# Optimization experiments

Measured on AMD Instinct MI355X. Metric: run time of the kernel, lower is better.

## Reference

```python
import jax, jax.numpy as jnp
import numpy as np

HIDDEN = 896
NUM_Q_HEADS = 14
NUM_KV_HEADS = 2
HEAD_DIM = 64
ROPE_BASE = 10000.0
B, S = 4, 2048


def rotate_half(x):
    x1, x2 = jnp.split(x, 2, axis=-1)
    return jnp.concatenate((-x2, x1), axis=-1)


def rope_cos_sin(position_ids):
    # position_ids: [B, S] int -> cos/sin [B, 1, S, HEAD_DIM]
    inv_freq = 1.0 / (ROPE_BASE ** (jnp.arange(0, HEAD_DIM, 2, dtype=jnp.float32) / HEAD_DIM))
    freqs = position_ids.astype(jnp.float32)[..., None] * inv_freq  # [B,S,D/2]
    emb = jnp.concatenate((freqs, freqs), axis=-1)  # [B,S,D]
    return jnp.cos(emb)[:, None, :, :], jnp.sin(emb)[:, None, :, :]


def setup_inputs() -> dict:
    key = jax.random.key(0)
    k1, k2, k3, k4, k5 = jax.random.split(key, 5)
    s = 1.0 / np.sqrt(HIDDEN)
    return {
        "hidden_states": jax.random.normal(k1, (B, S, HIDDEN), dtype=jnp.float32),
        "position_ids": jnp.broadcast_to(jnp.arange(S, dtype=jnp.int64), (B, S)),
        "Wq": jax.random.normal(k2, (HIDDEN, NUM_Q_HEADS * HEAD_DIM), dtype=jnp.float32) * s,
        "Wk": jax.random.normal(k3, (HIDDEN, NUM_KV_HEADS * HEAD_DIM), dtype=jnp.float32) * s,
        "Wv": jax.random.normal(k4, (HIDDEN, NUM_KV_HEADS * HEAD_DIM), dtype=jnp.float32) * s,
        "Wo": jax.random.normal(k5, (NUM_Q_HEADS * HEAD_DIM, HIDDEN), dtype=jnp.float32) * s,
    }


def reference(hidden_states, position_ids, Wq, Wk, Wv, Wo):
    b, s, _ = hidden_states.shape
    n_rep = NUM_Q_HEADS // NUM_KV_HEADS

    q = (hidden_states @ Wq).reshape(b, s, NUM_Q_HEADS, HEAD_DIM).transpose(0, 2, 1, 3)   # [B,Hq,S,D]
    k = (hidden_states @ Wk).reshape(b, s, NUM_KV_HEADS, HEAD_DIM).transpose(0, 2, 1, 3)  # [B,Hkv,S,D]
    v = (hidden_states @ Wv).reshape(b, s, NUM_KV_HEADS, HEAD_DIM).transpose(0, 2, 1, 3)

    cos, sin = rope_cos_sin(position_ids)  # [B,1,S,D]
    q = q * cos + rotate_half(q) * sin
    k = k * cos + rotate_half(k) * sin

    # repeat_interleave KV heads to match query heads
    k = jnp.repeat(k, n_rep, axis=1)  # [B,Hq,S,D]
    v = jnp.repeat(v, n_rep, axis=1)

    scale = 1.0 / jnp.sqrt(jnp.float32(HEAD_DIM))
    attn = jnp.einsum('bhqd,bhkd->bhqk', q, k) * scale  # [B,Hq,S,S]
    attn = jax.nn.softmax(attn, axis=-1)
    out = jnp.einsum('bhqk,bhkd->bhqd', attn, v)  # [B,Hq,S,D]
    out = out.transpose(0, 2, 1, 3).reshape(b, s, NUM_Q_HEADS * HEAD_DIM)
    return out @ Wo
```

## Files before the change

kernel.cpp:

```cpp
#include <hip/hip_runtime.h>
#include <hip/hip_bf16.h>
#include <math.h>

typedef unsigned short ushort_t;
typedef __bf16 bf16x8 __attribute__((ext_vector_type(8)));
typedef float f32x4 __attribute__((ext_vector_type(4)));

#define HIDDEN 896
#define NQH 14
#define NKVH 2
#define HD 64
#define SEQ 2048
#define NBATCH 4

__device__ inline ushort_t f2bf(float x) {
  union { float f; unsigned u; } c; c.f = x;
  unsigned r = c.u + 0x7FFFu + ((c.u >> 16) & 1u);
  return (ushort_t)(r >> 16);
}

__device__ inline unsigned pack2bf(float a, float b) {
  union { float f; unsigned u; } ca, cb; ca.f = a; cb.f = b;
  unsigned ua = ca.u + 0x8000u, ub = cb.u + 0x8000u;
  return __builtin_amdgcn_perm(ub, ua, 0x07060302);
}

__device__ inline bf16x8 ldfrag(const ushort_t* p) {
  return *reinterpret_cast<const bf16x8*>(p);
}

__device__ inline void async16(const ushort_t* g, ushort_t* l) {
  __builtin_amdgcn_global_load_lds(
      (const __attribute__((address_space(1))) void*)g,
      (__attribute__((address_space(3))) void*)l, 16, 0, 0);
}


__device__ inline void transpose_sec(const float* __restrict__ in, ushort_t* __restrict__ out,
                                     int K, int N, int bx, int by) {
  __shared__ float tile[32][33];
  int k0 = by * 32, n0 = bx * 32;
  for (int r = threadIdx.y; r < 32; r += 8) {
    int k = k0 + r, n = n0 + threadIdx.x;
    tile[r][threadIdx.x] = (k < K && n < N) ? in[(size_t)k * N + n] : 0.f;
  }
  __syncthreads();
  for (int r = threadIdx.y; r < 32; r += 8) {
    int n = n0 + r, k = k0 + threadIdx.x;
    if (n < N && k < K) out[(size_t)n * K + k] = f2bf(tile[threadIdx.x][r]);
  }
}

__global__ void k_prep(const float* __restrict__ hidden, ushort_t* __restrict__ hb,
                       const float* __restrict__ Wq, const float* __restrict__ Wk,
                       const float* __restrict__ Wv, const float* __restrict__ Wo,
                       ushort_t* __restrict__ wT, ushort_t* __restrict__ woT,
                       float2* __restrict__ ctab) {
  const int blk = blockIdx.x;
  const int tid = threadIdx.y * 32 + threadIdx.x;
  if (blk < 7168) {
    int i = blk * 256 + tid;
    float4 v = reinterpret_cast<const float4*>(hidden)[i];
    ushort4 o;
    o.x = f2bf(v.x); o.y = f2bf(v.y); o.z = f2bf(v.z); o.w = f2bf(v.w);
    reinterpret_cast<ushort4*>(hb)[i] = o;
  } else if (blk < 7424) {
    int idx = (blk - 7168) * 256 + tid;
    int s = idx >> 5, dp = idx & 31;
    float inv = exp2f(-(float)dp * 0.41524101186092596f);
    float ang = (float)s * inv;
    float sn, cn;
    sincosf(ang, &sn, &cn);
    ctab[idx] = make_float2(cn, sn);
  } else if (blk < 8208) {
    int t = blk - 7424;
    transpose_sec(Wq, wT, 896, 896, t % 28, t / 28);
  } else if (blk < 8320) {
    int t = blk - 8208;
    transpose_sec(Wk, wT + (size_t)896 * 896, 896, 128, t % 4, t / 4);
  } else if (blk < 8432) {
    int t = blk - 8320;
    transpose_sec(Wv, wT + (size_t)1024 * 896, 896, 128, t % 4, t / 4);
  } else {
    int t = blk - 8432;
    transpose_sec(Wo, woT, 896, 896, t % 28, t / 28);
  }
}

__global__ __launch_bounds__(256) void k_qkv(
    const ushort_t* __restrict__ hb,
    const ushort_t* __restrict__ wT,
    const int* __restrict__ pos_ids,
    const float2* __restrict__ ctab,
    ushort_t* __restrict__ Qg,
    ushort_t* __restrict__ Kg,
    ushort_t* __restrict__ Vtg) {
  __shared__ ushort_t smem[16384];
  ushort_t* sa = smem;
  ushort_t* sbb = smem + 8192;

  const int f = blockIdx.x;
  const int x = f & 7, s8 = f >> 3;
  const int sect = s8 % 9;
  const int mt = (s8 / 9) * 8 + x;
  const int nt0 = sect * 128;
  const int m0 = mt * 128;
  const int tid = threadIdx.x;
  const int wave = tid >> 6, lane = tid & 63;
  const int l15 = lane & 15, quad = lane >> 4;
  const int wm = wave >> 1, wn = wave & 1;
  const int sw = l15 & 7;

  f32x4 acc[4][4];
  const f32x4 z4 = {0.f, 0.f, 0.f, 0.f};
#pragma unroll
  for (int a = 0; a < 4; ++a)
#pragma unroll
    for (int b = 0; b < 4; ++b) acc[a][b] = z4;

  for (int kt = 0; kt < 14; ++kt) {
    const int k0 = kt * 64;
    __syncthreads();
#pragma unroll
    for (int i = 0; i < 4; ++i) {
      int id = i * 256 + tid;
      int row = id >> 3;
      int cs = (id & 7) ^ (row & 7);
      int base = (i * 256 + wave * 64) * 8;
      async16(hb + (size_t)(m0 + row) * HIDDEN + k0 + cs * 8, sa + base);
      async16(wT + (size_t)(nt0 + row) * HIDDEN + k0 + cs * 8, sbb + base);
    }
    __syncthreads();
    bf16x8 af[4][2], bf[4][2];
#pragma unroll
    for (int kc = 0; kc < 2; ++kc) {
      int c = kc * 4 + quad;
#pragma unroll
      for (int mb = 0; mb < 4; ++mb)
        af[mb][kc] = ldfrag(sa + ((wm * 64 + mb * 16 + l15) * 8 + (c ^ sw)) * 8);
#pragma unroll
      for (int nb = 0; nb < 4; ++nb)
        bf[nb][kc] = ldfrag(sbb + ((wn * 64 + nb * 16 + l15) * 8 + (c ^ sw)) * 8);
    }
#pragma unroll
    for (int mb = 0; mb < 4; ++mb)
#pragma unroll
      for (int nb = 0; nb < 4; ++nb) {
        acc[mb][nb] = __builtin_amdgcn_mfma_f32_16x16x32_bf16(af[mb][0], bf[nb][0], acc[mb][nb], 0, 0, 0);
        acc[mb][nb] = __builtin_amdgcn_mfma_f32_16x16x32_bf16(af[mb][1], bf[nb][1], acc[mb][nb], 0, 0, 0);
      }
  }

  if (sect < 8) {
    const bool isQ = sect < 7;
    const float csc = isQ ? 0.125f * 1.4426950408889634f : 1.0f;
    ushort_t* dst = isQ ? Qg : Kg;
    const int nheads = isQ ? NQH : NKVH;
    const int hh = isQ ? sect * 2 + wn : wn;
#pragma unroll
    for (int mb = 0; mb < 4; ++mb)
#pragma unroll
      for (int r = 0; r < 4; ++r) {
        int token = m0 + wm * 64 + mb * 16 + quad * 4 + r;
        int b = token >> 11, s = token & 2047;
        int pos = pos_ids[token];
        size_t base = ((size_t)(b * nheads + hh) * SEQ + s) * HD;
#pragma unroll
        for (int nb = 0; nb < 2; ++nb) {
          float2 cs = ctab[pos * 32 + nb * 16 + l15];
          float x0 = acc[mb][nb][r];
          float x1 = acc[mb][nb + 2][r];
          float y0 = (x0 * cs.x - x1 * cs.y) * csc;
          float y1 = (x1 * cs.x + x0 * cs.y) * csc;
          dst[base + nb * 16 + l15]      = f2bf(y0);
          dst[base + nb * 16 + l15 + 32] = f2bf(y1);
        }
      }
  } else {
    __syncthreads();
    ushort_t* vt = smem;
#pragma unroll
    for (int mb = 0; mb < 4; ++mb) {
      int tl = wm * 64 + mb * 16 + quad * 4;
      int chunk = tl >> 3, ofs = tl & 7;
#pragma unroll
      for (int nb = 0; nb < 4; ++nb) {
        int row = wn * 64 + nb * 16 + l15;
        int slot = chunk ^ (row & 7);
        ushort_t* p = vt + row * 128 + slot * 8 + ofs;
        *reinterpret_cast<unsigned*>(p)     = pack2bf(acc[mb][nb][0], acc[mb][nb][1]);
        *reinterpret_cast<unsigned*>(p + 2) = pack2bf(acc[mb][nb][2], acc[mb][nb][3]);
      }
    }
    __syncthreads();
    const int bb = m0 >> 11, s0 = m0 & 2047;
#pragma unroll
    for (int i = 0; i < 8; ++i) {
      int id = i * 256 + tid;
      int row = id >> 4, ch = id & 15;
      int kvh = row >> 6, d = row & 63;
      int slot = ch ^ (row & 7);
      uint4 v = *reinterpret_cast<const uint4*>(vt + row * 128 + slot * 8);
      *reinterpret_cast<uint4*>(Vtg + ((size_t)(bb * NKVH + kvh) * HD + d) * SEQ + s0 + ch * 8) = v;
    }
  }
}

__global__ __launch_bounds__(256) void k_attn(
    const ushort_t* __restrict__ Qg,
    const ushort_t* __restrict__ Kg,
    const ushort_t* __restrict__ Vtg,
    ushort_t* __restrict__ attn) {
  __shared__ ushort_t kbuf[64 * 64];
  __shared__ ushort_t vbuf[64 * 64];
  __shared__ ushort_t pbuf[4][64 * 72];

  const int f = blockIdx.x;
  const int x = f & 7, s8 = f >> 3;
  const int lh = s8 % 7;
  const int qt = s8 / 7;
  const int b = x >> 1, kvh = x & 1;
  const int h = kvh * 7 + lh;
  const int bh = b * NQH + h;
  const int tid = threadIdx.x;
  const int wave = tid >> 6, lane = tid & 63;
  const int l15 = lane & 15, quad = lane >> 4;
  const int sw = l15 & 7;
  const int q0 = qt * 256;

  bf16x8 qf[4][2];
#pragma unroll
  for (int qs = 0; qs < 4; ++qs) {
    const size_t qb = ((size_t)bh * SEQ + q0 + wave * 64 + qs * 16 + l15) * HD + quad * 8;
    qf[qs][0] = ldfrag(Qg + qb);
    qf[qs][1] = ldfrag(Qg + qb + 32);
  }

  const size_t kbase = (size_t)(b * NKVH + kvh) * SEQ * HD;
  const size_t vbase = (size_t)(b * NKVH + kvh) * HD * SEQ;

  const int srow = tid >> 3;
  const int sc0 = (tid & 7) ^ (srow & 7);
  const int srow2 = (256 + tid) >> 3;
  const int sc2 = (tid & 7) ^ (srow2 & 7);
  const int sbase1 = wave * 64 * 8;
  const int sbase2 = (256 + wave * 64) * 8;

  float lsum[4] = {0.f, 0.f, 0.f, 0.f};
  f32x4 o[4][4];
  const f32x4 z4 = {0.f, 0.f, 0.f, 0.f};
#pragma unroll
  for (int qs = 0; qs < 4; ++qs)
#pragma unroll
    for (int nb = 0; nb < 4; ++nb) o[qs][nb] = z4;

  ushort_t* pw = pbuf[wave];

  for (int jt = 0; jt < 32; ++jt) {
    const int s0 = jt * 64;
    __syncthreads();
    async16(Kg + kbase + (size_t)(s0 + srow) * HD + sc0 * 8, kbuf + sbase1);
    async16(Vtg + vbase + (size_t)srow * SEQ + s0 + sc0 * 8, vbuf + sbase1);
    async16(Kg + kbase + (size_t)(s0 + srow2) * HD + sc2 * 8, kbuf + sbase2);
    async16(Vtg + vbase + (size_t)srow2 * SEQ + s0 + sc2 * 8, vbuf + sbase2);
    __syncthreads();

#pragma unroll
    for (int nb = 0; nb < 4; ++nb) {
      int row = nb * 16 + l15;
      bf16x8 kf0 = ldfrag(kbuf + (row * 8 + (quad ^ sw)) * 8);
      bf16x8 kf1 = ldfrag(kbuf + (row * 8 + ((4 + quad) ^ sw)) * 8);
#pragma unroll
      for (int qs = 0; qs < 4; ++qs) {
        f32x4 t = z4;
        t = __builtin_amdgcn_mfma_f32_16x16x32_bf16(kf0, qf[qs][0], t, 0, 0, 0);
        t = __builtin_amdgcn_mfma_f32_16x16x32_bf16(kf1, qf[qs][1], t, 0, 0, 0);
        float p0 = __builtin_amdgcn_exp2f(t[0]);
        float p1 = __builtin_amdgcn_exp2f(t[1]);
        float p2 = __builtin_amdgcn_exp2f(t[2]);
        float p3 = __builtin_amdgcn_exp2f(t[3]);
        lsum[qs] += (p0 + p1) + (p2 + p3);
        uint2 d;
        d.x = pack2bf(p0, p1);
        d.y = pack2bf(p2, p3);
        *reinterpret_cast<uint2*>(pw + (qs * 16 + l15) * 72 + nb * 16 + quad * 4) = d;
      }
    }

    bf16x8 pf[4][2];
#pragma unroll
    for (int qs = 0; qs < 4; ++qs) {
      pf[qs][0] = ldfrag(pw + (qs * 16 + l15) * 72 + quad * 8);
      pf[qs][1] = ldfrag(pw + (qs * 16 + l15) * 72 + 32 + quad * 8);
    }
#pragma unroll
    for (int nb = 0; nb < 4; ++nb) {
      int row = nb * 16 + l15;
      bf16x8 vf0 = ldfrag(vbuf + (row * 8 + (quad ^ sw)) * 8);
      bf16x8 vf1 = ldfrag(vbuf + (row * 8 + ((4 + quad) ^ sw)) * 8);
#pragma unroll
      for (int qs = 0; qs < 4; ++qs) {
        o[qs][nb] = __builtin_amdgcn_mfma_f32_16x16x32_bf16(pf[qs][0], vf0, o[qs][nb], 0, 0, 0);
        o[qs][nb] = __builtin_amdgcn_mfma_f32_16x16x32_bf16(pf[qs][1], vf1, o[qs][nb], 0, 0, 0);
      }
    }
  }

#pragma unroll
  for (int qs = 0; qs < 4; ++qs) {
    float s = lsum[qs];
    s += __shfl_xor(s, 16);
    s += __shfl_xor(s, 32);
    lsum[qs] = 1.0f / s;
  }

#pragma unroll
  for (int qs = 0; qs < 4; ++qs) {
#pragma unroll
    for (int r = 0; r < 4; ++r) {
      float inv = __shfl(lsum[qs], quad * 4 + r);
      int qg = q0 + wave * 64 + qs * 16 + quad * 4 + r;
#pragma unroll
      for (int nb = 0; nb < 4; ++nb) {
        float val = o[qs][nb][r] * inv;
        attn[(size_t)(b * SEQ + qg) * (NQH * HD) + h * HD + nb * 16 + l15] = f2bf(val);
      }
    }
  }
}

__global__ __launch_bounds__(256) void k_oproj(
    const ushort_t* __restrict__ attn,
    const ushort_t* __restrict__ woT,
    float* __restrict__ out) {
  __shared__ ushort_t smem[16384];
  ushort_t* sa = smem;
  ushort_t* sbb = smem + 8192;

  const int f = blockIdx.x;
  const int x = f & 7, s8 = f >> 3;
  const int n_sect = s8 % 7;
  const int mt = (s8 / 7) * 8 + x;
  const int n0 = n_sect * 128;
  const int m0 = mt * 128;
  const int tid = threadIdx.x;
  const int wave = tid >> 6, lane = tid & 63;
  const int l15 = lane & 15, quad = lane >> 4;
  const int wm = wave >> 1, wn = wave & 1;
  const int sw = l15 & 7;

  f32x4 acc[4][4];
  const f32x4 z4 = {0.f, 0.f, 0.f, 0.f};
#pragma unroll
  for (int a = 0; a < 4; ++a)
#pragma unroll
    for (int b = 0; b < 4; ++b) acc[a][b] = z4;

  for (int kt = 0; kt < 14; ++kt) {
    const int k0 = kt * 64;
    __syncthreads();
#pragma unroll
    for (int i = 0; i < 4; ++i) {
      int id = i * 256 + tid;
      int row = id >> 3;
      int cs = (id & 7) ^ (row & 7);
      int base = (i * 256 + wave * 64) * 8;
      async16(attn + (size_t)(m0 + row) * HIDDEN + k0 + cs * 8, sa + base);
      async16(woT + (size_t)(n0 + row) * HIDDEN + k0 + cs * 8, sbb + base);
    }
    __syncthreads();
    bf16x8 af[4][2], bf[4][2];
#pragma unroll
    for (int kc = 0; kc < 2; ++kc) {
      int c = kc * 4 + quad;
#pragma unroll
      for (int mb = 0; mb < 4; ++mb)
        af[mb][kc] = ldfrag(sa + ((wm * 64 + mb * 16 + l15) * 8 + (c ^ sw)) * 8);
#pragma unroll
      for (int nb = 0; nb < 4; ++nb)
        bf[nb][kc] = ldfrag(sbb + ((wn * 64 + nb * 16 + l15) * 8 + (c ^ sw)) * 8);
    }
#pragma unroll
    for (int mb = 0; mb < 4; ++mb)
#pragma unroll
      for (int nb = 0; nb < 4; ++nb) {
        acc[mb][nb] = __builtin_amdgcn_mfma_f32_16x16x32_bf16(af[mb][0], bf[nb][0], acc[mb][nb], 0, 0, 0);
        acc[mb][nb] = __builtin_amdgcn_mfma_f32_16x16x32_bf16(af[mb][1], bf[nb][1], acc[mb][nb], 0, 0, 0);
      }
  }

#pragma unroll
  for (int mb = 0; mb < 4; ++mb)
#pragma unroll
    for (int nb = 0; nb < 4; ++nb)
#pragma unroll
      for (int r = 0; r < 4; ++r)
        out[(size_t)(m0 + wm * 64 + mb * 16 + quad * 4 + r) * HIDDEN +
            n0 + wn * 64 + nb * 16 + l15] = acc[mb][nb][r];
}


extern "C" void kernel_launch(void* const* d_in, const int* in_sizes, int n_in,
                              void* d_out, int out_size, void* d_ws, size_t ws_size,
                              hipStream_t stream) {
  (void)in_sizes; (void)n_in; (void)out_size; (void)ws_size;
  const float* hidden = (const float*)d_in[0];
  const int* pos      = (const int*)d_in[1];
  const float* Wq     = (const float*)d_in[2];
  const float* Wk     = (const float*)d_in[3];
  const float* Wv     = (const float*)d_in[4];
  const float* Wo     = (const float*)d_in[5];
  float* out = (float*)d_out;

  char* ws = (char*)d_ws;
  ushort_t* hb   = (ushort_t*)(ws);
  ushort_t* wT   = (ushort_t*)(ws + 14680064);
  float2*   ctab = (float2*)  (ws + 16744448);
  ushort_t* Qg   = (ushort_t*)(ws + 17268736);
  ushort_t* Kg   = (ushort_t*)(ws + 31948800);
  ushort_t* Vtg  = (ushort_t*)(ws + 34045952);
  ushort_t* attn = (ushort_t*)(ws + 36143104);
  ushort_t* woT  = (ushort_t*)(ws + 50823168);

  k_prep<<<9216, dim3(32, 8), 0, stream>>>(hidden, hb, Wq, Wk, Wv, Wo, wT, woT, ctab);
  k_qkv<<<576, 256, 0, stream>>>(hb, wT, pos, ctab, Qg, Kg, Vtg);
  k_attn<<<448, 256, 0, stream>>>(Qg, Kg, Vtg, attn);
  k_oproj<<<448, 256, 0, stream>>>(attn, woT, out);
}
```

Baseline: 277.4 us.

## Use single-wave attention blocks loading K/V fragments directly from global memory

Restructures the attention kernel from 256-thread blocks that stage K and V tiles in shared memory into 64-thread single-wave blocks, launching 1792 blocks instead of 448. Each wave now loads its K and V MFMA fragments straight from global memory (relying on cache), which removes the block-wide __syncthreads barriers and the shared staging. The softmax row sum is now computed with MFMA against a ones vector rather than scalar adds and shuffles. The cost is that the seven query waves sharing a KV head no longer share one staged copy, so K/V global and cache traffic rises.

```diff
diff --git a/kernel.cpp b/kernel.cpp
--- a/kernel.cpp
+++ b/kernel.cpp
@@ -206,70 +206,57 @@
   }
 }
 
-__global__ __launch_bounds__(256) void k_attn(
+__global__ __launch_bounds__(64, 2) void k_attn(
     const ushort_t* __restrict__ Qg,
     const ushort_t* __restrict__ Kg,
     const ushort_t* __restrict__ Vtg,
     ushort_t* __restrict__ attn) {
-  __shared__ ushort_t kbuf[64 * 64];
-  __shared__ ushort_t vbuf[64 * 64];
-  __shared__ ushort_t pbuf[4][64 * 72];
+  __shared__ ushort_t pbuf[64 * 72];
 
   const int f = blockIdx.x;
   const int x = f & 7, s8 = f >> 3;
   const int lh = s8 % 7;
-  const int qt = s8 / 7;
+  const int qc = s8 / 7;
   const int b = x >> 1, kvh = x & 1;
   const int h = kvh * 7 + lh;
   const int bh = b * NQH + h;
-  const int tid = threadIdx.x;
-  const int wave = tid >> 6, lane = tid & 63;
+  const int lane = threadIdx.x;
   const int l15 = lane & 15, quad = lane >> 4;
-  const int sw = l15 & 7;
-  const int q0 = qt * 256;
+  const int q0 = qc * 64;
 
   bf16x8 qf[4][2];
 #pragma unroll
   for (int qs = 0; qs < 4; ++qs) {
-    const size_t qb = ((size_t)bh * SEQ + q0 + wave * 64 + qs * 16 + l15) * HD + quad * 8;
+    const size_t qb = ((size_t)bh * SEQ + q0 + qs * 16 + l15) * HD + quad * 8;
     qf[qs][0] = ldfrag(Qg + qb);
     qf[qs][1] = ldfrag(Qg + qb + 32);
   }
 
-  const size_t kbase = (size_t)(b * NKVH + kvh) * SEQ * HD;
-  const size_t vbase = (size_t)(b * NKVH + kvh) * HD * SEQ;
-
-  const int srow = tid >> 3;
-  const int sc0 = (tid & 7) ^ (srow & 7);
-  const int srow2 = (256 + tid) >> 3;
-  const int sc2 = (tid & 7) ^ (srow2 & 7);
-  const int sbase1 = wave * 64 * 8;
-  const int sbase2 = (256 + wave * 64) * 8;
-
-  float lsum[4] = {0.f, 0.f, 0.f, 0.f};
+  bf16x8 ones;
+#pragma unroll
+  for (int i = 0; i < 8; ++i) ones[i] = (__bf16)1.0f;
+
+  const ushort_t* Kb = Kg + (size_t)(b * NKVH + kvh) * SEQ * HD;
+  const ushort_t* Vb = Vtg + (size_t)(b * NKVH + kvh) * HD * SEQ;
+
   f32x4 o[4][4];
+  f32x4 lfr[4];
   const f32x4 z4 = {0.f, 0.f, 0.f, 0.f};
 #pragma unroll
-  for (int qs = 0; qs < 4; ++qs)
+  for (int qs = 0; qs < 4; ++qs) {
+    lfr[qs] = z4;
 #pragma unroll
     for (int nb = 0; nb < 4; ++nb) o[qs][nb] = z4;
-
-  ushort_t* pw = pbuf[wave];
+  }
 
   for (int jt = 0; jt < 32; ++jt) {
     const int s0 = jt * 64;
-    __syncthreads();
-    async16(Kg + kbase + (size_t)(s0 + srow) * HD + sc0 * 8, kbuf + sbase1);
-    async16(Vtg + vbase + (size_t)srow * SEQ + s0 + sc0 * 8, vbuf + sbase1);
-    async16(Kg + kbase + (size_t)(s0 + srow2) * HD + sc2 * 8, kbuf + sbase2);
-    async16(Vtg + vbase + (size_t)srow2 * SEQ + s0 + sc2 * 8, vbuf + sbase2);
-    __syncthreads();
 
 #pragma unroll
     for (int nb = 0; nb < 4; ++nb) {
-      int row = nb * 16 + l15;
-      bf16x8 kf0 = ldfrag(kbuf + (row * 8 + (quad ^ sw)) * 8);
-      bf16x8 kf1 = ldfrag(kbuf + (row * 8 + ((4 + quad) ^ sw)) * 8);
+      const ushort_t* kr = Kb + (size_t)(s0 + nb * 16 + l15) * HD + quad * 8;
+      bf16x8 kf0 = ldfrag(kr);
+      bf16x8 kf1 = ldfrag(kr + 32);
 #pragma unroll
       for (int qs = 0; qs < 4; ++qs) {
         f32x4 t = z4;
@@ -279,25 +266,27 @@
         float p1 = __builtin_amdgcn_exp2f(t[1]);
         float p2 = __builtin_amdgcn_exp2f(t[2]);
         float p3 = __builtin_amdgcn_exp2f(t[3]);
-        lsum[qs] += (p0 + p1) + (p2 + p3);
         uint2 d;
         d.x = pack2bf(p0, p1);
         d.y = pack2bf(p2, p3);
-        *reinterpret_cast<uint2*>(pw + (qs * 16 + l15) * 72 + nb * 16 + quad * 4) = d;
+        *reinterpret_cast<uint2*>(pbuf + (qs * 16 + l15) * 72 + nb * 16 + quad * 4) = d;
       }
     }
 
     bf16x8 pf[4][2];
 #pragma unroll
     for (int qs = 0; qs < 4; ++qs) {
-      pf[qs][0] = ldfrag(pw + (qs * 16 + l15) * 72 + quad * 8);
-      pf[qs][1] = ldfrag(pw + (qs * 16 + l15) * 72 + 32 + quad * 8);
-    }
+      pf[qs][0] = ldfrag(pbuf + (qs * 16 + l15) * 72 + quad * 8);
+      pf[qs][1] = ldfrag(pbuf + (qs * 16 + l15) * 72 + 32 + quad * 8);
+      lfr[qs] = __builtin_amdgcn_mfma_f32_16x16x32_bf16(pf[qs][0], ones, lfr[qs], 0, 0, 0);
+      lfr[qs] = __builtin_amdgcn_mfma_f32_16x16x32_bf16(pf[qs][1], ones, lfr[qs], 0, 0, 0);
+    }
+
 #pragma unroll
     for (int nb = 0; nb < 4; ++nb) {
-      int row = nb * 16 + l15;
-      bf16x8 vf0 = ldfrag(vbuf + (row * 8 + (quad ^ sw)) * 8);
-      bf16x8 vf1 = ldfrag(vbuf + (row * 8 + ((4 + quad) ^ sw)) * 8);
+      const ushort_t* vr = Vb + (size_t)(nb * 16 + l15) * SEQ + s0 + quad * 8;
+      bf16x8 vf0 = ldfrag(vr);
+      bf16x8 vf1 = ldfrag(vr + 32);
 #pragma unroll
       for (int qs = 0; qs < 4; ++qs) {
         o[qs][nb] = __builtin_amdgcn_mfma_f32_16x16x32_bf16(pf[qs][0], vf0, o[qs][nb], 0, 0, 0);
@@ -308,18 +297,10 @@
 
 #pragma unroll
   for (int qs = 0; qs < 4; ++qs) {
-    float s = lsum[qs];
-    s += __shfl_xor(s, 16);
-    s += __shfl_xor(s, 32);
-    lsum[qs] = 1.0f / s;
-  }
-
-#pragma unroll
-  for (int qs = 0; qs < 4; ++qs) {
 #pragma unroll
     for (int r = 0; r < 4; ++r) {
-      float inv = __shfl(lsum[qs], quad * 4 + r);
-      int qg = q0 + wave * 64 + qs * 16 + quad * 4 + r;
+      float inv = __builtin_amdgcn_rcpf(lfr[qs][r]);
+      int qg = q0 + qs * 16 + quad * 4 + r;
 #pragma unroll
       for (int nb = 0; nb < 4; ++nb) {
         float val = o[qs][nb][r] * inv;
@@ -424,6 +405,6 @@
 
   k_prep<<<9216, dim3(32, 8), 0, stream>>>(hidden, hb, Wq, Wk, Wv, Wo, wT, woT, ctab);
   k_qkv<<<576, 256, 0, stream>>>(hb, wT, pos, ctab, Qg, Kg, Vtg);
-  k_attn<<<448, 256, 0, stream>>>(Qg, Kg, Vtg, attn);
+  k_attn<<<1792, 64, 0, stream>>>(Qg, Kg, Vtg, attn);
   k_oproj<<<448, 256, 0, stream>>>(attn, woT, out);
 }
```

Result: faster. 254.9 us (-8.1%).
